# Kernel tuning notes

Measured on AMD Instinct MI355X. Metric: run time of the kernel, lower is better.

The kernel has to match this reference:

```python
import jax, jax.numpy as jnp
import numpy as np

B, S, D_MODEL, D_KEY = 4, 2048, 1024, 128


def setup_inputs() -> dict:
    key = jax.random.key(0)
    kq, kk, kv, kwq, kwk, kwv = jax.random.split(key, 6)
    queries = jax.random.normal(kq, (B, S, D_MODEL), dtype=jnp.float32)
    keys = jax.random.normal(kk, (B, S, D_MODEL), dtype=jnp.float32)
    values = jax.random.normal(kv, (B, S, D_MODEL), dtype=jnp.float32)
    # causal mask: 1 where attention is allowed (j <= i), 0 otherwise
    mask = jnp.broadcast_to(jnp.tril(jnp.ones((S, S), dtype=jnp.int32)), (B, S, S))
    # torch nn.Linear weights are [out, in]; init ~ U(-1/sqrt(in), 1/sqrt(in))
    bound = 1.0 / np.sqrt(D_MODEL)
    Wq = jax.random.uniform(kwq, (D_KEY, D_MODEL), jnp.float32, -bound, bound)
    Wk = jax.random.uniform(kwk, (D_KEY, D_MODEL), jnp.float32, -bound, bound)
    Wv = jax.random.uniform(kwv, (D_KEY, D_MODEL), jnp.float32, -bound, bound)
    return {"queries": queries, "keys": keys, "values": values, "mask": mask,
            "Wq": Wq, "Wk": Wk, "Wv": Wv}


def reference(queries, keys, values, mask, Wq, Wk, Wv):
    d_key = Wq.shape[0]
    q = jnp.einsum('bsd,kd->bsk', queries, Wq)   # [B,S,d_key]
    k = jnp.einsum('bsd,kd->bsk', keys, Wk)
    v = jnp.einsum('bsd,kd->bsk', values, Wv)
    attn = jnp.einsum('bqk,bsk->bqs', q, k) / jnp.sqrt(jnp.float32(d_key))  # [B,S,S]
    attn = jnp.where(mask == 0, -jnp.inf, attn)
    attn = jax.nn.softmax(attn, axis=-1)
    return jnp.einsum('bqs,bsk->bqk', attn, v)   # [B,S,d_key]
```

## Files before the change

kernel.cpp:

```cpp
#include <hip/hip_runtime.h>
#include <hip/hip_bf16.h>

#define NB 4
#define SEQ 2048
#define DMODEL 1024
#define DKEY 128

using f32x4  = __attribute__((ext_vector_type(4))) float;
using bf16x8 = __attribute__((ext_vector_type(8))) short;
using u16x4  = __attribute__((ext_vector_type(4))) unsigned short;
using u16x8  = __attribute__((ext_vector_type(8))) unsigned short;

__device__ __forceinline__ unsigned short f2bf(float f) {
  __hip_bfloat16 h = __float2bfloat16(f);
  return __builtin_bit_cast(unsigned short, h);
}

__global__ __launch_bounds__(256) void proj_kernel(
    const float* __restrict__ Xq, const float* __restrict__ Xk, const float* __restrict__ Xv,
    const float* __restrict__ Wq, const float* __restrict__ Wk, const float* __restrict__ Wv,
    unsigned short* __restrict__ Yq, unsigned short* __restrict__ Yk,
    unsigned short* __restrict__ Vt)
{
  const int z = blockIdx.z;
  const float* X = (z == 0) ? Xq : (z == 1) ? Xk : Xv;
  const float* W = (z == 0) ? Wq : (z == 1) ? Wk : Wv;

  __shared__ alignas(16) unsigned short Xl[2][64][40];
  __shared__ alignas(16) unsigned short Wl[2][128][40];
  __shared__ alignas(16) unsigned short Tl[128][72];

  const int t     = threadIdx.x;
  const int lane  = t & 63;
  const int w     = t >> 6;
  const int lr    = lane & 15;
  const int lk    = (lane >> 4) * 8;
  const int rbase = (lane >> 4) * 4;
  const long m0   = (long)blockIdx.x * 64;

  f32x4 acc[8];
  const f32x4 zero = {0.f, 0.f, 0.f, 0.f};
#pragma unroll
  for (int n = 0; n < 8; ++n) acc[n] = zero;

  float4 xr[2], wr[4];
#pragma unroll
  for (int i = 0; i < 2; ++i) {
    int id = t + 256 * i, row = id >> 3, c4 = (id & 7) << 2;
    xr[i] = *reinterpret_cast<const float4*>(&X[(m0 + row) * DMODEL + c4]);
  }
#pragma unroll
  for (int i = 0; i < 4; ++i) {
    int id = t + 256 * i, row = id >> 3, c4 = (id & 7) << 2;
    wr[i] = *reinterpret_cast<const float4*>(&W[(long)row * DMODEL + c4]);
  }

  for (int ks = 0; ks < DMODEL / 32; ++ks) {
    const int cur = ks & 1;
#pragma unroll
    for (int i = 0; i < 2; ++i) {
      int id = t + 256 * i, row = id >> 3, c4 = (id & 7) << 2;
      u16x4 p = { f2bf(xr[i].x), f2bf(xr[i].y), f2bf(xr[i].z), f2bf(xr[i].w) };
      *reinterpret_cast<u16x4*>(&Xl[cur][row][c4]) = p;
    }
#pragma unroll
    for (int i = 0; i < 4; ++i) {
      int id = t + 256 * i, row = id >> 3, c4 = (id & 7) << 2;
      u16x4 p = { f2bf(wr[i].x), f2bf(wr[i].y), f2bf(wr[i].z), f2bf(wr[i].w) };
      *reinterpret_cast<u16x4*>(&Wl[cur][row][c4]) = p;
    }
    if (ks + 1 < DMODEL / 32) {
      const int k0 = (ks + 1) * 32;
#pragma unroll
      for (int i = 0; i < 2; ++i) {
        int id = t + 256 * i, row = id >> 3, c4 = (id & 7) << 2;
        xr[i] = *reinterpret_cast<const float4*>(&X[(m0 + row) * DMODEL + k0 + c4]);
      }
#pragma unroll
      for (int i = 0; i < 4; ++i) {
        int id = t + 256 * i, row = id >> 3, c4 = (id & 7) << 2;
        wr[i] = *reinterpret_cast<const float4*>(&W[(long)row * DMODEL + k0 + c4]);
      }
    }
    __syncthreads();

    bf16x8 a = *reinterpret_cast<const bf16x8*>(&Xl[cur][w * 16 + lr][lk]);
#pragma unroll
    for (int n = 0; n < 8; ++n) {
      bf16x8 b = *reinterpret_cast<const bf16x8*>(&Wl[cur][n * 16 + lr][lk]);
      acc[n] = __builtin_amdgcn_mfma_f32_16x16x32_bf16(a, b, acc[n], 0, 0, 0);
    }
  }

  if (z != 2) {
    unsigned short* Y = (z == 0) ? Yq : Yk;
#pragma unroll
    for (int n = 0; n < 8; ++n)
#pragma unroll
      for (int r = 0; r < 4; ++r) {
        long row = m0 + w * 16 + rbase + r;
        Y[row * DKEY + n * 16 + lr] = f2bf(acc[n][r]);
      }
  } else {
#pragma unroll
    for (int n = 0; n < 8; ++n)
#pragma unroll
      for (int r = 0; r < 4; ++r)
        Tl[n * 16 + lr][w * 16 + rbase + r] = f2bf(acc[n][r]);
    __syncthreads();
    const int bb = (int)(m0 >> 11);
    const int s0 = (int)(m0 & 2047);
#pragma unroll
    for (int i = 0; i < 4; ++i) {
      int id = t + 256 * i;
      int dr = id >> 3;
      int c8 = (id & 7) << 3;
      u16x8 v = *reinterpret_cast<const u16x8*>(&Tl[dr][c8]);
      *reinterpret_cast<u16x8*>(&Vt[((size_t)bb * DKEY + dr) * SEQ + s0 + c8]) = v;
    }
  }
}

__global__ __launch_bounds__(512, 2) void attn_kernel(
    const unsigned short* __restrict__ Q,
    const unsigned short* __restrict__ K,
    const unsigned short* __restrict__ Vt,
    float* __restrict__ O)
{
  const int  L    = blockIdx.x;
  const int  b    = (L & 7) >> 1;
  const int  qt   = 63 - (((L >> 3) << 1) | (L & 1));
  const int  q0   = qt * 32;
  const long base = (long)b * SEQ;
  const int  nt   = (q0 >> 6) + 1;
  const int  nsteps = (nt + 3) >> 2;

  __shared__ alignas(16) unsigned short Kl[4][64][128];
  __shared__ alignas(16) unsigned short Vl[4][128][64];
  __shared__ alignas(16) unsigned short Plds[8][16][72];
  __shared__ float Sm[4][32], Sl[4][32];

  const int t     = threadIdx.x;
  const int lane  = t & 63;
  const int w     = t >> 6;
  const int g     = w >> 1;
  const int wq    = w & 1;
  const int lr    = lane & 15;
  const int hi    = lane >> 4;
  const int lk    = hi * 8;
  const int rbase = hi * 4;

  bf16x8 qa[4];
  {
    const long qrow = (base + q0 + wq * 16 + lr) * (long)DKEY;
#pragma unroll
    for (int dk = 0; dk < 4; ++dk)
      qa[dk] = *reinterpret_cast<const bf16x8*>(&Q[qrow + dk * 32 + lk]);
  }

  const f32x4 zero = {0.f, 0.f, 0.f, 0.f};
  f32x4 oacc[8];
#pragma unroll
  for (int n = 0; n < 8; ++n) oacc[n] = zero;
  float m_run[4], l_run[4];
#pragma unroll
  for (int r = 0; r < 4; ++r) { m_run[r] = -1e30f; l_run[r] = 0.0f; }

  const float sc = 0.08838834764831845f;
  const unsigned short* VtB = Vt + (size_t)b * DKEY * SEQ;

  for (int st = 0; st < nsteps; ++st) {
    const int kt  = st * 4 + g;
    const bool act = kt < nt;
    const int kv0 = kt * 64;

    if (act) {
      const unsigned short* Kp = K + (base + kv0) * (long)DKEY;
#pragma unroll
      for (int it = 0; it < 8; ++it) {
        int c = it * 128 + wq * 64 + lane;
        int row = c >> 4, sl = (c & 15) ^ (row & 7);
        *reinterpret_cast<u16x8*>(&Kl[g][row][sl * 8]) =
            *reinterpret_cast<const u16x8*>(&Kp[(size_t)c * 8]);
      }
#pragma unroll
      for (int it = 0; it < 8; ++it) {
        int c = it * 128 + wq * 64 + lane;
        int d = c >> 3, sl = c & 7, slp = sl ^ (d & 7);
        *reinterpret_cast<u16x8*>(&Vl[g][d][slp * 8]) =
            *reinterpret_cast<const u16x8*>(&VtB[(size_t)d * SEQ + kv0 + sl * 8]);
      }
    }
    __syncthreads();

    if (act) {
      f32x4 s[4];
#pragma unroll
      for (int kc = 0; kc < 4; ++kc) {
        s[kc] = zero;
#pragma unroll
        for (int dk = 0; dk < 4; ++dk) {
          bf16x8 kb = *reinterpret_cast<const bf16x8*>(
              &Kl[g][kc * 16 + lr][((dk * 4 + hi) ^ (lr & 7)) * 8]);
          s[kc] = __builtin_amdgcn_mfma_f32_16x16x32_bf16(qa[dk], kb, s[kc], 0, 0, 0);
        }
      }

      const bool dmask = (kt == nt - 1);
      float x[4][4];
#pragma unroll
      for (int kc = 0; kc < 4; ++kc)
#pragma unroll
        for (int r = 0; r < 4; ++r) {
          float xv = s[kc][r] * sc;
          if (dmask) {
            int col  = kv0 + kc * 16 + lr;
            int rowq = q0 + wq * 16 + rbase + r;
            if (col > rowq) xv = -1e30f;
          }
          x[kc][r] = xv;
        }

#pragma unroll
      for (int r = 0; r < 4; ++r) {
        float tm = fmaxf(fmaxf(x[0][r], x[1][r]), fmaxf(x[2][r], x[3][r]));
        tm = fmaxf(tm, __shfl_xor(tm, 1));
        tm = fmaxf(tm, __shfl_xor(tm, 2));
        tm = fmaxf(tm, __shfl_xor(tm, 4));
        tm = fmaxf(tm, __shfl_xor(tm, 8));
        float mnew = fmaxf(m_run[r], tm);
        float scl  = __expf(m_run[r] - mnew);
        m_run[r] = mnew;
        float ps = 0.0f;
#pragma unroll
        for (int kc = 0; kc < 4; ++kc) {
          float pp = __expf(x[kc][r] - mnew);
          ps += pp;
          Plds[w][rbase + r][kc * 16 + lr] = f2bf(pp);
        }
        ps += __shfl_xor(ps, 1);
        ps += __shfl_xor(ps, 2);
        ps += __shfl_xor(ps, 4);
        ps += __shfl_xor(ps, 8);
        l_run[r] = l_run[r] * scl + ps;
#pragma unroll
        for (int n = 0; n < 8; ++n) oacc[n][r] *= scl;
      }

#pragma unroll
      for (int kk = 0; kk < 2; ++kk) {
        bf16x8 pa = *reinterpret_cast<const bf16x8*>(&Plds[w][lr][kk * 32 + lk]);
#pragma unroll
        for (int n = 0; n < 8; ++n) {
          bf16x8 vb = *reinterpret_cast<const bf16x8*>(
              &Vl[g][n * 16 + lr][((kk * 4 + hi) ^ (lr & 7)) * 8]);
          oacc[n] = __builtin_amdgcn_mfma_f32_16x16x32_bf16(pa, vb, oacc[n], 0, 0, 0);
        }
      }
    }
    __syncthreads();
  }

  float* Om = reinterpret_cast<float*>(&Kl[0][0][0]);
#pragma unroll
  for (int n = 0; n < 8; ++n)
#pragma unroll
    for (int r = 0; r < 4; ++r)
      Om[(g * 32 + wq * 16 + rbase + r) * 128 + n * 16 + lr] = oacc[n][r];
  if (lr == 0) {
#pragma unroll
    for (int r = 0; r < 4; ++r) {
      Sm[g][wq * 16 + rbase + r] = m_run[r];
      Sl[g][wq * 16 + rbase + r] = l_run[r];
    }
  }
  __syncthreads();

  const int row = t >> 4;
  const int c0  = (t & 15) * 8;
  float mM = fmaxf(fmaxf(Sm[0][row], Sm[1][row]), fmaxf(Sm[2][row], Sm[3][row]));
  float wts[4], lsum = 0.0f;
#pragma unroll
  for (int gv = 0; gv < 4; ++gv) {
    wts[gv] = __expf(Sm[gv][row] - mM);
    lsum += wts[gv] * Sl[gv][row];
  }
  const float linv = 1.0f / lsum;
  f32x4 o0 = zero, o1 = zero;
#pragma unroll
  for (int gv = 0; gv < 4; ++gv) {
    const float* src = &Om[(gv * 32 + row) * 128 + c0];
    f32x4 a0 = *reinterpret_cast<const f32x4*>(src);
    f32x4 a1 = *reinterpret_cast<const f32x4*>(src + 4);
    const float wt = wts[gv];
#pragma unroll
    for (int j = 0; j < 4; ++j) { o0[j] += wt * a0[j]; o1[j] += wt * a1[j]; }
  }
#pragma unroll
  for (int j = 0; j < 4; ++j) { o0[j] *= linv; o1[j] *= linv; }
  float* op = &O[(base + q0 + row) * (long)DKEY + c0];
  *reinterpret_cast<f32x4*>(op)     = o0;
  *reinterpret_cast<f32x4*>(op + 4) = o1;
}

extern "C" void kernel_launch(void* const* d_in, const int* in_sizes, int n_in,
                              void* d_out, int out_size, void* d_ws, size_t ws_size,
                              hipStream_t stream) {
  const float* Xq = (const float*)d_in[0];
  const float* Xk = (const float*)d_in[1];
  const float* Xv = (const float*)d_in[2];
  const float* Wq = (const float*)d_in[4];
  const float* Wk = (const float*)d_in[5];
  const float* Wv = (const float*)d_in[6];

  unsigned short* qp  = (unsigned short*)d_ws;
  unsigned short* kp  = qp + (size_t)NB * SEQ * DKEY;
  unsigned short* vtp = kp + (size_t)NB * SEQ * DKEY;

  dim3 g1(SEQ * NB / 64, 1, 3);
  hipLaunchKernelGGL(proj_kernel, g1, dim3(256), 0, stream,
                     Xq, Xk, Xv, Wq, Wk, Wv, qp, kp, vtp);
  hipLaunchKernelGGL(attn_kernel, dim3(256), dim3(512), 0, stream,
                     qp, kp, vtp, (float*)d_out);
}
```

Baseline: 61.49 us.

## Pre-convert weights to bf16 and load projection MFMA fragments directly from global

Adds a small kernel that converts Wq/Wk/Wv to bf16 once per call, storing the result temporarily in the output buffer. The projection kernel no longer stages tiles through LDS. Each wave now loads its A (fp32 X, packed to bf16 in registers) and B (bf16 W) fragments straight from global memory, using a 2x2 wave tiling and register double-buffering in place of LDS staging and per-step barriers. This removes per-block fp32 weight conversion, the LDS traffic and the syncthreads. The cost is an extra launch and uncoalesced, fragment-shaped global loads that depend on the cache to absorb the redundancy.

```diff
diff --git a/kernel.cpp b/kernel.cpp
--- a/kernel.cpp
+++ b/kernel.cpp
@@ -15,98 +15,116 @@
   __hip_bfloat16 h = __float2bfloat16(f);
   return __builtin_bit_cast(unsigned short, h);
 }
-
-__global__ __launch_bounds__(256) void proj_kernel(
+__device__ __forceinline__ bf16x8 pack8(float4 lo, float4 hi) {
+  u16x8 p = { f2bf(lo.x), f2bf(lo.y), f2bf(lo.z), f2bf(lo.w),
+              f2bf(hi.x), f2bf(hi.y), f2bf(hi.z), f2bf(hi.w) };
+  return __builtin_bit_cast(bf16x8, p);
+}
+
+__global__ __launch_bounds__(256) void wconv_kernel(
+    const float* __restrict__ Wq, const float* __restrict__ Wk,
+    const float* __restrict__ Wv, unsigned short* __restrict__ Wb)
+{
+  int id = blockIdx.x * 256 + threadIdx.x;
+  const float* src = (id < 16384) ? Wq : (id < 32768) ? Wk : Wv;
+  int off = (id & 16383) * 8;
+  float4 a = *reinterpret_cast<const float4*>(&src[off]);
+  float4 b = *reinterpret_cast<const float4*>(&src[off + 4]);
+  u16x8 p = { f2bf(a.x), f2bf(a.y), f2bf(a.z), f2bf(a.w),
+              f2bf(b.x), f2bf(b.y), f2bf(b.z), f2bf(b.w) };
+  *reinterpret_cast<u16x8*>(&Wb[(size_t)(id >> 14) * 131072 + off]) = p;
+}
+
+__global__ __launch_bounds__(256, 1) void proj_kernel(
     const float* __restrict__ Xq, const float* __restrict__ Xk, const float* __restrict__ Xv,
-    const float* __restrict__ Wq, const float* __restrict__ Wk, const float* __restrict__ Wv,
+    const unsigned short* __restrict__ Wb,
     unsigned short* __restrict__ Yq, unsigned short* __restrict__ Yk,
     unsigned short* __restrict__ Vt)
 {
   const int z = blockIdx.z;
   const float* X = (z == 0) ? Xq : (z == 1) ? Xk : Xv;
-  const float* W = (z == 0) ? Wq : (z == 1) ? Wk : Wv;
-
-  __shared__ alignas(16) unsigned short Xl[2][64][40];
-  __shared__ alignas(16) unsigned short Wl[2][128][40];
+  const unsigned short* W = Wb + (size_t)z * 131072;
+
   __shared__ alignas(16) unsigned short Tl[128][72];
 
-  const int t     = threadIdx.x;
-  const int lane  = t & 63;
-  const int w     = t >> 6;
-  const int lr    = lane & 15;
-  const int lk    = (lane >> 4) * 8;
-  const int rbase = (lane >> 4) * 4;
-  const long m0   = (long)blockIdx.x * 64;
-
-  f32x4 acc[8];
+  const int t    = threadIdx.x;
+  const int lane = t & 63;
+  const int w    = t >> 6;
+  const int wm   = w >> 1;
+  const int wn   = w & 1;
+  const int lr   = lane & 15;
+  const int hi   = lane >> 4;
+  const int lk   = hi * 8;
+  const int rbase = hi * 4;
+  const long m0  = (long)blockIdx.x * 64;
+
+  const float* pA0 = X + (m0 + wm * 32 + 0  + lr) * (long)DMODEL + lk;
+  const float* pA1 = X + (m0 + wm * 32 + 16 + lr) * (long)DMODEL + lk;
+  const unsigned short* pB0 = W + (wn * 64 + 0  + lr) * DMODEL + lk;
+  const unsigned short* pB1 = W + (wn * 64 + 16 + lr) * DMODEL + lk;
+  const unsigned short* pB2 = W + (wn * 64 + 32 + lr) * DMODEL + lk;
+  const unsigned short* pB3 = W + (wn * 64 + 48 + lr) * DMODEL + lk;
+
+  f32x4 acc[2][4];
   const f32x4 zero = {0.f, 0.f, 0.f, 0.f};
 #pragma unroll
-  for (int n = 0; n < 8; ++n) acc[n] = zero;
-
-  float4 xr[2], wr[4];
-#pragma unroll
-  for (int i = 0; i < 2; ++i) {
-    int id = t + 256 * i, row = id >> 3, c4 = (id & 7) << 2;
-    xr[i] = *reinterpret_cast<const float4*>(&X[(m0 + row) * DMODEL + c4]);
-  }
-#pragma unroll
-  for (int i = 0; i < 4; ++i) {
-    int id = t + 256 * i, row = id >> 3, c4 = (id & 7) << 2;
-    wr[i] = *reinterpret_cast<const float4*>(&W[(long)row * DMODEL + c4]);
-  }
-
-  for (int ks = 0; ks < DMODEL / 32; ++ks) {
-    const int cur = ks & 1;
-#pragma unroll
-    for (int i = 0; i < 2; ++i) {
-      int id = t + 256 * i, row = id >> 3, c4 = (id & 7) << 2;
-      u16x4 p = { f2bf(xr[i].x), f2bf(xr[i].y), f2bf(xr[i].z), f2bf(xr[i].w) };
-      *reinterpret_cast<u16x4*>(&Xl[cur][row][c4]) = p;
-    }
-#pragma unroll
-    for (int i = 0; i < 4; ++i) {
-      int id = t + 256 * i, row = id >> 3, c4 = (id & 7) << 2;
-      u16x4 p = { f2bf(wr[i].x), f2bf(wr[i].y), f2bf(wr[i].z), f2bf(wr[i].w) };
-      *reinterpret_cast<u16x4*>(&Wl[cur][row][c4]) = p;
-    }
-    if (ks + 1 < DMODEL / 32) {
-      const int k0 = (ks + 1) * 32;
-#pragma unroll
-      for (int i = 0; i < 2; ++i) {
-        int id = t + 256 * i, row = id >> 3, c4 = (id & 7) << 2;
-        xr[i] = *reinterpret_cast<const float4*>(&X[(m0 + row) * DMODEL + k0 + c4]);
-      }
-#pragma unroll
-      for (int i = 0; i < 4; ++i) {
-        int id = t + 256 * i, row = id >> 3, c4 = (id & 7) << 2;
-        wr[i] = *reinterpret_cast<const float4*>(&W[(long)row * DMODEL + k0 + c4]);
-      }
-    }
-    __syncthreads();
-
-    bf16x8 a = *reinterpret_cast<const bf16x8*>(&Xl[cur][w * 16 + lr][lk]);
-#pragma unroll
-    for (int n = 0; n < 8; ++n) {
-      bf16x8 b = *reinterpret_cast<const bf16x8*>(&Wl[cur][n * 16 + lr][lk]);
-      acc[n] = __builtin_amdgcn_mfma_f32_16x16x32_bf16(a, b, acc[n], 0, 0, 0);
-    }
-  }
+  for (int m = 0; m < 2; ++m)
+#pragma unroll
+    for (int n = 0; n < 4; ++n) acc[m][n] = zero;
+
+  float4 xa[2][4];
+  bf16x8 wf[2][4];
+
+#define PJ_LOAD(rg, ks) do {                                                  \
+    xa[rg][0] = *reinterpret_cast<const float4*>(pA0 + (ks) * 32);            \
+    xa[rg][1] = *reinterpret_cast<const float4*>(pA0 + (ks) * 32 + 4);        \
+    xa[rg][2] = *reinterpret_cast<const float4*>(pA1 + (ks) * 32);            \
+    xa[rg][3] = *reinterpret_cast<const float4*>(pA1 + (ks) * 32 + 4);        \
+    wf[rg][0] = *reinterpret_cast<const bf16x8*>(pB0 + (ks) * 32);            \
+    wf[rg][1] = *reinterpret_cast<const bf16x8*>(pB1 + (ks) * 32);            \
+    wf[rg][2] = *reinterpret_cast<const bf16x8*>(pB2 + (ks) * 32);            \
+    wf[rg][3] = *reinterpret_cast<const bf16x8*>(pB3 + (ks) * 32);            \
+  } while (0)
+
+#define PJ_COMP(rg) do {                                                      \
+    bf16x8 a0 = pack8(xa[rg][0], xa[rg][1]);                                  \
+    bf16x8 a1 = pack8(xa[rg][2], xa[rg][3]);                                  \
+    _Pragma("unroll")                                                         \
+    for (int n = 0; n < 4; ++n) {                                             \
+      acc[0][n] = __builtin_amdgcn_mfma_f32_16x16x32_bf16(a0, wf[rg][n], acc[0][n], 0, 0, 0); \
+      acc[1][n] = __builtin_amdgcn_mfma_f32_16x16x32_bf16(a1, wf[rg][n], acc[1][n], 0, 0, 0); \
+    }                                                                         \
+  } while (0)
+
+  PJ_LOAD(0, 0);
+  for (int ks = 0; ks < 32; ks += 2) {
+    PJ_LOAD(1, ks + 1);
+    PJ_COMP(0);
+    if (ks + 2 < 32) PJ_LOAD(0, ks + 2);
+    PJ_COMP(1);
+  }
+#undef PJ_LOAD
+#undef PJ_COMP
 
   if (z != 2) {
     unsigned short* Y = (z == 0) ? Yq : Yk;
 #pragma unroll
-    for (int n = 0; n < 8; ++n)
-#pragma unroll
-      for (int r = 0; r < 4; ++r) {
-        long row = m0 + w * 16 + rbase + r;
-        Y[row * DKEY + n * 16 + lr] = f2bf(acc[n][r]);
-      }
+    for (int m = 0; m < 2; ++m)
+#pragma unroll
+      for (int n = 0; n < 4; ++n)
+#pragma unroll
+        for (int r = 0; r < 4; ++r) {
+          long row = m0 + wm * 32 + m * 16 + rbase + r;
+          Y[row * DKEY + wn * 64 + n * 16 + lr] = f2bf(acc[m][n][r]);
+        }
   } else {
 #pragma unroll
-    for (int n = 0; n < 8; ++n)
-#pragma unroll
-      for (int r = 0; r < 4; ++r)
-        Tl[n * 16 + lr][w * 16 + rbase + r] = f2bf(acc[n][r]);
+    for (int m = 0; m < 2; ++m)
+#pragma unroll
+      for (int n = 0; n < 4; ++n)
+#pragma unroll
+        for (int r = 0; r < 4; ++r)
+          Tl[wn * 64 + n * 16 + lr][wm * 32 + m * 16 + rbase + r] = f2bf(acc[m][n][r]);
     __syncthreads();
     const int bb = (int)(m0 >> 11);
     const int s0 = (int)(m0 & 2047);
@@ -316,10 +334,13 @@
   unsigned short* qp  = (unsigned short*)d_ws;
   unsigned short* kp  = qp + (size_t)NB * SEQ * DKEY;
   unsigned short* vtp = kp + (size_t)NB * SEQ * DKEY;
-
+  unsigned short* wbp = (unsigned short*)d_out;
+
+  hipLaunchKernelGGL(wconv_kernel, dim3(192), dim3(256), 0, stream,
+                     Wq, Wk, Wv, wbp);
   dim3 g1(SEQ * NB / 64, 1, 3);
   hipLaunchKernelGGL(proj_kernel, g1, dim3(256), 0, stream,
-                     Xq, Xk, Xv, Wq, Wk, Wv, qp, kp, vtp);
+                     Xq, Xk, Xv, wbp, qp, kp, vtp);
   hipLaunchKernelGGL(attn_kernel, dim3(256), dim3(512), 0, stream,
                      qp, kp, vtp, (float*)d_out);
 }
```

Result: slower. 100.7 us (+63.7%).

## Pre-convert weights to bf16 and stream projection tiles via async global-to-LDS loads

Applied to the files above, without the earlier changes.

Adds a small kernel that converts Wq/Wk/Wv to bf16 once per call into scratch space in the output buffer. The projection kernel then uses global_load_lds direct-to-LDS copies with a triple-buffered pipeline and XOR-swizzled layouts. X stays fp32 in LDS and is packed to bf16 at fragment-read time. This is meant to remove register staging, per-iteration conversion of weights and the full barrier stall, so loads overlap the MFMAs. The cost is an extra launch and higher LDS use, and correctness depends on the output buffer being used as scratch before attention overwrites it.

```diff
diff --git a/kernel.cpp b/kernel.cpp
--- a/kernel.cpp
+++ b/kernel.cpp
@@ -15,82 +15,100 @@
   __hip_bfloat16 h = __float2bfloat16(f);
   return __builtin_bit_cast(unsigned short, h);
 }
-
-__global__ __launch_bounds__(256) void proj_kernel(
+__device__ __forceinline__ bf16x8 pack8(f32x4 lo, f32x4 hi) {
+  u16x8 p = { f2bf(lo[0]), f2bf(lo[1]), f2bf(lo[2]), f2bf(lo[3]),
+              f2bf(hi[0]), f2bf(hi[1]), f2bf(hi[2]), f2bf(hi[3]) };
+  return __builtin_bit_cast(bf16x8, p);
+}
+__device__ __forceinline__ void gload16(const void* g, void* l) {
+  __builtin_amdgcn_global_load_lds(
+      (const __attribute__((address_space(1))) void*)g,
+      (__attribute__((address_space(3))) void*)l, 16, 0, 0);
+}
+
+__global__ __launch_bounds__(256) void wconv_kernel(
+    const float* __restrict__ Wq, const float* __restrict__ Wk,
+    const float* __restrict__ Wv, unsigned short* __restrict__ Wb)
+{
+  int id = blockIdx.x * 256 + threadIdx.x;
+  const float* src = (id < 16384) ? Wq : (id < 32768) ? Wk : Wv;
+  int off = (id & 16383) * 8;
+  float4 a = *reinterpret_cast<const float4*>(&src[off]);
+  float4 b = *reinterpret_cast<const float4*>(&src[off + 4]);
+  u16x8 p = { f2bf(a.x), f2bf(a.y), f2bf(a.z), f2bf(a.w),
+              f2bf(b.x), f2bf(b.y), f2bf(b.z), f2bf(b.w) };
+  *reinterpret_cast<u16x8*>(&Wb[(size_t)(id >> 14) * 131072 + off]) = p;
+}
+
+__global__ __launch_bounds__(256, 2) void proj_kernel(
     const float* __restrict__ Xq, const float* __restrict__ Xk, const float* __restrict__ Xv,
-    const float* __restrict__ Wq, const float* __restrict__ Wk, const float* __restrict__ Wv,
+    const unsigned short* __restrict__ Wb,
     unsigned short* __restrict__ Yq, unsigned short* __restrict__ Yk,
     unsigned short* __restrict__ Vt)
 {
   const int z = blockIdx.z;
   const float* X = (z == 0) ? Xq : (z == 1) ? Xk : Xv;
-  const float* W = (z == 0) ? Wq : (z == 1) ? Wk : Wv;
-
-  __shared__ alignas(16) unsigned short Xl[2][64][40];
-  __shared__ alignas(16) unsigned short Wl[2][128][40];
+  const unsigned short* W = Wb + (size_t)z * 131072;
+
+  __shared__ alignas(16) float          XL[3][64 * 32];
+  __shared__ alignas(16) unsigned short WL[3][128 * 32];
   __shared__ alignas(16) unsigned short Tl[128][72];
 
   const int t     = threadIdx.x;
   const int lane  = t & 63;
   const int w     = t >> 6;
   const int lr    = lane & 15;
-  const int lk    = (lane >> 4) * 8;
-  const int rbase = (lane >> 4) * 4;
+  const int hi    = lane >> 4;
+  const int rbase = hi * 4;
   const long m0   = (long)blockIdx.x * 64;
+
+  const int xg_row[2] = { (0 * 256 + t) >> 3, (1 * 256 + t) >> 3 };
+  const int xg_col[2] = { ((((0 * 256 + t) & 7) ^ (xg_row[0] & 7)) << 2),
+                          ((((1 * 256 + t) & 7) ^ (xg_row[1] & 7)) << 2) };
+  const int wg_row[2] = { (0 * 256 + t) >> 2, (1 * 256 + t) >> 2 };
+  const int wg_col[2] = { ((((0 * 256 + t) & 3) ^ (wg_row[0] & 3)) << 3),
+                          ((((1 * 256 + t) & 3) ^ (wg_row[1] & 3)) << 3) };
+
+#define PJ_ISSUE(ks) do {                                                     \
+    const int _b = (ks) % 3;                                                  \
+    _Pragma("unroll")                                                         \
+    for (int i = 0; i < 2; ++i) {                                             \
+      gload16(&X[(m0 + xg_row[i]) * (long)DMODEL + (ks) * 32 + xg_col[i]],    \
+              &XL[_b][(i * 256 + w * 64) * 4]);                               \
+      gload16(&W[(size_t)wg_row[i] * DMODEL + (ks) * 32 + wg_col[i]],         \
+              &WL[_b][(i * 256 + w * 64) * 8]);                               \
+    }                                                                         \
+  } while (0)
 
   f32x4 acc[8];
   const f32x4 zero = {0.f, 0.f, 0.f, 0.f};
 #pragma unroll
   for (int n = 0; n < 8; ++n) acc[n] = zero;
 
-  float4 xr[2], wr[4];
-#pragma unroll
-  for (int i = 0; i < 2; ++i) {
-    int id = t + 256 * i, row = id >> 3, c4 = (id & 7) << 2;
-    xr[i] = *reinterpret_cast<const float4*>(&X[(m0 + row) * DMODEL + c4]);
-  }
-#pragma unroll
-  for (int i = 0; i < 4; ++i) {
-    int id = t + 256 * i, row = id >> 3, c4 = (id & 7) << 2;
-    wr[i] = *reinterpret_cast<const float4*>(&W[(long)row * DMODEL + c4]);
-  }
-
-  for (int ks = 0; ks < DMODEL / 32; ++ks) {
-    const int cur = ks & 1;
-#pragma unroll
-    for (int i = 0; i < 2; ++i) {
-      int id = t + 256 * i, row = id >> 3, c4 = (id & 7) << 2;
-      u16x4 p = { f2bf(xr[i].x), f2bf(xr[i].y), f2bf(xr[i].z), f2bf(xr[i].w) };
-      *reinterpret_cast<u16x4*>(&Xl[cur][row][c4]) = p;
-    }
-#pragma unroll
-    for (int i = 0; i < 4; ++i) {
-      int id = t + 256 * i, row = id >> 3, c4 = (id & 7) << 2;
-      u16x4 p = { f2bf(wr[i].x), f2bf(wr[i].y), f2bf(wr[i].z), f2bf(wr[i].w) };
-      *reinterpret_cast<u16x4*>(&Wl[cur][row][c4]) = p;
-    }
-    if (ks + 1 < DMODEL / 32) {
-      const int k0 = (ks + 1) * 32;
-#pragma unroll
-      for (int i = 0; i < 2; ++i) {
-        int id = t + 256 * i, row = id >> 3, c4 = (id & 7) << 2;
-        xr[i] = *reinterpret_cast<const float4*>(&X[(m0 + row) * DMODEL + k0 + c4]);
-      }
-#pragma unroll
-      for (int i = 0; i < 4; ++i) {
-        int id = t + 256 * i, row = id >> 3, c4 = (id & 7) << 2;
-        wr[i] = *reinterpret_cast<const float4*>(&W[(long)row * DMODEL + k0 + c4]);
-      }
-    }
-    __syncthreads();
-
-    bf16x8 a = *reinterpret_cast<const bf16x8*>(&Xl[cur][w * 16 + lr][lk]);
+  PJ_ISSUE(0);
+  PJ_ISSUE(1);
+
+  const int arow = w * 16 + lr;
+  for (int ks = 0; ks < 32; ++ks) {
+    if (ks < 31) asm volatile("s_waitcnt vmcnt(4)" ::: "memory");
+    else         asm volatile("s_waitcnt vmcnt(0)" ::: "memory");
+    __builtin_amdgcn_s_barrier();
+    if (ks + 2 < 32) PJ_ISSUE(ks + 2);
+
+    const int buf = ks % 3;
+    const float* xrow = &XL[buf][arow * 32];
+    f32x4 xlo = *reinterpret_cast<const f32x4*>(xrow + (((hi * 2)     ^ (lr & 7)) << 2));
+    f32x4 xhi = *reinterpret_cast<const f32x4*>(xrow + (((hi * 2 + 1) ^ (lr & 7)) << 2));
+    bf16x8 a = pack8(xlo, xhi);
 #pragma unroll
     for (int n = 0; n < 8; ++n) {
-      bf16x8 b = *reinterpret_cast<const bf16x8*>(&Wl[cur][n * 16 + lr][lk]);
+      const int wrow = n * 16 + lr;
+      bf16x8 b = *reinterpret_cast<const bf16x8*>(
+          &WL[buf][wrow * 32 + ((hi ^ (wrow & 3)) << 3)]);
       acc[n] = __builtin_amdgcn_mfma_f32_16x16x32_bf16(a, b, acc[n], 0, 0, 0);
     }
   }
+#undef PJ_ISSUE
 
   if (z != 2) {
     unsigned short* Y = (z == 0) ? Yq : Yk;
@@ -102,6 +120,7 @@
         Y[row * DKEY + n * 16 + lr] = f2bf(acc[n][r]);
       }
   } else {
+    __syncthreads();
 #pragma unroll
     for (int n = 0; n < 8; ++n)
 #pragma unroll
@@ -316,10 +335,13 @@
   unsigned short* qp  = (unsigned short*)d_ws;
   unsigned short* kp  = qp + (size_t)NB * SEQ * DKEY;
   unsigned short* vtp = kp + (size_t)NB * SEQ * DKEY;
-
+  unsigned short* wbp = (unsigned short*)d_out;
+
+  hipLaunchKernelGGL(wconv_kernel, dim3(192), dim3(256), 0, stream,
+                     Wq, Wk, Wv, wbp);
   dim3 g1(SEQ * NB / 64, 1, 3);
   hipLaunchKernelGGL(proj_kernel, g1, dim3(256), 0, stream,
-                     Xq, Xk, Xv, Wq, Wk, Wv, qp, kp, vtp);
+                     Xq, Xk, Xv, wbp, qp, kp, vtp);
   hipLaunchKernelGGL(attn_kernel, dim3(256), dim3(512), 0, stream,
                      qp, kp, vtp, (float*)d_out);
 }
```

New measurement: 66.54 us. 8.2% more time.
